# Kernel tuning notes

Hardware: AMD Instinct MI355X
Metric: run time of the kernel (lower is better)

Reference implementation:

```python
import jax, jax.numpy as jnp
import numpy as np


def setup_inputs() -> dict:
    key = jax.random.key(0)
    kW, kH, kT = jax.random.split(key, 3)
    N, M, rank = 1024, 1024, 64
    W = jax.random.uniform(kW, (N, rank), dtype=jnp.float32)
    H = jax.random.uniform(kH, (rank, M), dtype=jnp.float32)
    tau = jax.random.uniform(kT, (N, rank), dtype=jnp.float32)
    return {"W": W, "H": H, "tau": tau}


def reference(W, H, tau):
    # Vectorized ShiftNMF forward over all M frequency bins at once.
    # Original: for f in range(M): WHt[:, f] = (softplus(W) * exp(-1j*2*pi*f/M * tau)) @ Hf[:, f]
    M = H.shape[1]
    Hf = jnp.fft.fft(jax.nn.softplus(H), axis=1)          # (rank, M) complex64
    Wp = jax.nn.softplus(W)                                # (N, rank)
    freqs = jnp.arange(M, dtype=jnp.float32)               # (M,)
    # phase[n, r, f] = exp(-1j * 2*pi*f/M * tau[n, r])
    phase = jnp.exp((-2j * jnp.pi / M) * tau[:, :, None] * freqs[None, None, :])  # (N, rank, M)
    # WHt[n, f] = sum_r Wp[n, r] * phase[n, r, f] * Hf[r, f]
    WHt = jnp.einsum('nr,nrf,rf->nf', Wp.astype(phase.dtype), phase, Hf)
    return WHt
```

## Files before the change

### kernel.cpp

```cpp
#include <hip/hip_runtime.h>
#include <math.h>

#define M_DIM 1024
#define N_DIM 1024
#define NRANK 64
#define BN 16
#define BF 64

__device__ float g_HfRe[NRANK * M_DIM];
__device__ float g_HfIm[NRANK * M_DIM];

__device__ __forceinline__ float softplus_f(float x) {
    return log1pf(__expf(x));
}

__device__ __forceinline__ float fast_sin_rev(float rev) {
#if __has_builtin(__builtin_amdgcn_sinf)
    return __builtin_amdgcn_sinf(rev);
#else
    return __sinf(rev * 6.28318530717958647f);
#endif
}
__device__ __forceinline__ float fast_cos_rev(float rev) {
#if __has_builtin(__builtin_amdgcn_cosf)
    return __builtin_amdgcn_cosf(rev);
#else
    return __cosf(rev * 6.28318530717958647f);
#endif
}

__global__ __launch_bounds__(512) void fft_rows(const float* __restrict__ H) {
    __shared__ float sre[M_DIM];
    __shared__ float sim[M_DIM];
    const int r = blockIdx.x;
    const int tid = threadIdx.x;

    for (int j = tid; j < M_DIM; j += 512) {
        int src = __brev((unsigned)j) >> 22;
        sre[j] = softplus_f(H[r * M_DIM + src]);
        sim[j] = 0.0f;
    }
    __syncthreads();

    int log2half = 0;
    for (int len = 2; len <= M_DIM; len <<= 1, ++log2half) {
        const int half = len >> 1;
        const int j    = tid & (half - 1);
        const int base = (tid >> log2half) << (log2half + 1);
        const int i0   = base + j;
        const int i1   = i0 + half;
        const float rev = -(float)j / (float)len;
        const float s = fast_sin_rev(rev);
        const float c = fast_cos_rev(rev);
        const float xr = sre[i1], xi = sim[i1];
        const float vr = xr * c - xi * s;
        const float vi = xr * s + xi * c;
        const float ur = sre[i0], ui = sim[i0];
        sre[i0] = ur + vr;  sim[i0] = ui + vi;
        sre[i1] = ur - vr;  sim[i1] = ui - vi;
        __syncthreads();
    }

    for (int j = tid; j < M_DIM; j += 512) {
        g_HfRe[r * M_DIM + j] = sre[j];
        g_HfIm[r * M_DIM + j] = sim[j];
    }
}

__global__ __launch_bounds__(256) void shiftnmf_main(
    const float* __restrict__ W, const float* __restrict__ tau,
    float* __restrict__ out, int out_elems) {

    __shared__ float shHr[NRANK][BF];
    __shared__ float shHi[NRANK][BF];
    __shared__ float shWp[BN][NRANK];
    __shared__ float shA [BN][NRANK];

    const int tid = threadIdx.x;
    const int f0  = blockIdx.x * BF;
    const int n0  = blockIdx.y * BN;

    for (int idx = tid; idx < NRANK * BF; idx += 256) {
        const int rr = idx >> 6, ff = idx & 63;
        shHr[rr][ff] = g_HfRe[rr * M_DIM + f0 + ff];
        shHi[rr][ff] = g_HfIm[rr * M_DIM + f0 + ff];
    }
    for (int idx = tid; idx < BN * NRANK; idx += 256) {
        const int nn = idx >> 6, rr = idx & 63;
        const int n  = n0 + nn;
        shWp[nn][rr] = softplus_f(W[n * NRANK + rr]);
        shA [nn][rr] = (-1.0f / (float)M_DIM) * tau[n * NRANK + rr];
    }
    __syncthreads();

    const int ff  = tid & 63;
    const int ni0 = tid >> 6;
    const float fglob = (float)(f0 + ff);

    float accRe[4] = {0.f, 0.f, 0.f, 0.f};
    float accIm[4] = {0.f, 0.f, 0.f, 0.f};

    for (int r = 0; r < NRANK; ++r) {
        const float hr = shHr[r][ff];
        const float hi = shHi[r][ff];
        #pragma unroll
        for (int k = 0; k < 4; ++k) {
            const int nn = ni0 + (k << 2);
            const float wp = shWp[nn][r];
            const float a  = shA [nn][r];
            const float rev = a * fglob;
            const float s = fast_sin_rev(rev);
            const float c = fast_cos_rev(rev);
            const float wr = wp * hr;
            const float wi = wp * hi;
            accRe[k] = fmaf(c, wr, fmaf(-s, wi, accRe[k]));
            accIm[k] = fmaf(c, wi, fmaf( s, wr, accIm[k]));
        }
    }

    #pragma unroll
    for (int k = 0; k < 4; ++k) {
        const int n  = n0 + ni0 + (k << 2);
        const int oi = n * M_DIM + f0 + ff;
        if (oi < out_elems) out[oi] = accRe[k];
        const int oj = N_DIM * M_DIM + oi;
        if (oj < out_elems) out[oj] = accIm[k];
    }
}

extern "C" void kernel_launch(void* const* d_in, const int* in_sizes, int n_in,
                              void* d_out, int out_size, void* d_ws, size_t ws_size,
                              hipStream_t stream) {
    const float* W   = (const float*)d_in[0];
    const float* H   = (const float*)d_in[1];
    const float* tau = (const float*)d_in[2];

    (void)d_ws; (void)ws_size;

    fft_rows<<<NRANK, 512, 0, stream>>>(H);
    shiftnmf_main<<<dim3(M_DIM / BF, N_DIM / BN), 256, 0, stream>>>(
        W, tau, (float*)d_out, out_size);
}
```

Measured before the change: 88.33 us.

## Replace per-element sincos with phase-rotation recurrence across frequency strides

Each thread now owns one row n and four frequencies spaced 16 apart, instead of one frequency and four rows. It computes sin/cos once per rank and steps the phase forward by multiplying with a precomputed rotation exp(-2πi·16·a), replacing three of every four transcendental evaluations with complex multiplies. The W/tau shared arrays are transposed to rank-major so each rank reads its row entries contiguously. This trades transcendental throughput for extra FMAs and adds some accumulated rounding error from the recurrence. Output stores become strided per thread, which may reduce write coalescing.

Result: no change. 86.85 us (-1.7%).

```diff
diff --git a/kernel.cpp b/kernel.cpp
--- a/kernel.cpp
+++ b/kernel.cpp
@@ -73,8 +73,10 @@
 
     __shared__ float shHr[NRANK][BF];
     __shared__ float shHi[NRANK][BF];
-    __shared__ float shWp[BN][NRANK];
-    __shared__ float shA [BN][NRANK];
+    __shared__ float shWp[NRANK][BN];
+    __shared__ float shA [NRANK][BN];
+    __shared__ float shSc[NRANK][BN];
+    __shared__ float shSs[NRANK][BN];
 
     const int tid = threadIdx.x;
     const int f0  = blockIdx.x * BF;
@@ -88,40 +90,51 @@
     for (int idx = tid; idx < BN * NRANK; idx += 256) {
         const int nn = idx >> 6, rr = idx & 63;
         const int n  = n0 + nn;
-        shWp[nn][rr] = softplus_f(W[n * NRANK + rr]);
-        shA [nn][rr] = (-1.0f / (float)M_DIM) * tau[n * NRANK + rr];
+        const float wp = softplus_f(W[n * NRANK + rr]);
+        const float a  = (-1.0f / (float)M_DIM) * tau[n * NRANK + rr];
+        shWp[rr][nn] = wp;
+        shA [rr][nn] = a;
+        const float rev16 = a * 16.0f;
+        shSc[rr][nn] = fast_cos_rev(rev16);
+        shSs[rr][nn] = fast_sin_rev(rev16);
     }
     __syncthreads();
 
-    const int ff  = tid & 63;
-    const int ni0 = tid >> 6;
-    const float fglob = (float)(f0 + ff);
+    const int fbase = tid & 15;
+    const int n_loc = tid >> 4;
+    const float fglob = (float)(f0 + fbase);
 
     float accRe[4] = {0.f, 0.f, 0.f, 0.f};
     float accIm[4] = {0.f, 0.f, 0.f, 0.f};
 
     for (int r = 0; r < NRANK; ++r) {
-        const float hr = shHr[r][ff];
-        const float hi = shHi[r][ff];
+        const float wp  = shWp[r][n_loc];
+        const float a   = shA [r][n_loc];
+        const float c16 = shSc[r][n_loc];
+        const float s16 = shSs[r][n_loc];
+        const float rev0 = a * fglob;
+        const float s0 = fast_sin_rev(rev0);
+        const float c0 = fast_cos_rev(rev0);
+        float pr = wp * c0;
+        float pi = wp * s0;
         #pragma unroll
         for (int k = 0; k < 4; ++k) {
-            const int nn = ni0 + (k << 2);
-            const float wp = shWp[nn][r];
-            const float a  = shA [nn][r];
-            const float rev = a * fglob;
-            const float s = fast_sin_rev(rev);
-            const float c = fast_cos_rev(rev);
-            const float wr = wp * hr;
-            const float wi = wp * hi;
-            accRe[k] = fmaf(c, wr, fmaf(-s, wi, accRe[k]));
-            accIm[k] = fmaf(c, wi, fmaf( s, wr, accIm[k]));
+            const float hr = shHr[r][fbase + (k << 4)];
+            const float hi = shHi[r][fbase + (k << 4)];
+            accRe[k] = fmaf(pr, hr, fmaf(-pi, hi, accRe[k]));
+            accIm[k] = fmaf(pr, hi, fmaf( pi, hr, accIm[k]));
+            if (k < 3) {
+                const float npr = fmaf(pr, c16, -pi * s16);
+                pi = fmaf(pr, s16, pi * c16);
+                pr = npr;
+            }
         }
     }
 
     #pragma unroll
     for (int k = 0; k < 4; ++k) {
-        const int n  = n0 + ni0 + (k << 2);
-        const int oi = n * M_DIM + f0 + ff;
+        const int n  = n0 + n_loc;
+        const int oi = n * M_DIM + f0 + fbase + (k << 4);
         if (oi < out_elems) out[oi] = accRe[k];
         const int oj = N_DIM * M_DIM + oi;
         if (oj < out_elems) out[oj] = accIm[k];
```
